# Performance work log

Hardware: AMD Instinct MI355X
Metric: run time of the kernel (lower is better)

The kernel has to match this reference:

```python
import jax, jax.numpy as jnp
import numpy as np

D_IN = 1024
D_OUT = 1024
NUM_HEADS = 16
HEAD_DIM = D_OUT // NUM_HEADS


def setup_inputs() -> dict:
    key = jax.random.key(0)
    ks = jax.random.split(key, 6)
    scale = 0.02
    x = jax.random.normal(ks[0], (4, 2048, D_IN), dtype=jnp.float32)
    Wq = jax.random.normal(ks[1], (D_IN, D_OUT), dtype=jnp.float32) * scale
    Wk = jax.random.normal(ks[2], (D_IN, D_OUT), dtype=jnp.float32) * scale
    Wv = jax.random.normal(ks[3], (D_IN, D_OUT), dtype=jnp.float32) * scale
    Wo = jax.random.normal(ks[4], (D_OUT, D_OUT), dtype=jnp.float32) * scale
    bo = jax.random.normal(ks[5], (D_OUT,), dtype=jnp.float32) * scale
    return {"x": x, "Wq": Wq, "Wk": Wk, "Wv": Wv, "Wo": Wo, "bo": bo}


def reference(x, Wq, Wk, Wv, Wo, bo):
    b, n, _ = x.shape
    # QKV projections -> [b, h, n, hd]
    def split_heads(t):
        return t.reshape(b, n, NUM_HEADS, HEAD_DIM).transpose(0, 2, 1, 3)
    q = split_heads(x @ Wq)
    k = split_heads(x @ Wk)
    v = split_heads(x @ Wv)
    # scaled causal attention scores [b, h, n, n]
    scores = jnp.einsum('bhqd,bhkd->bhqk', q, k) / jnp.sqrt(jnp.float32(HEAD_DIM))
    causal = jnp.tril(jnp.ones((n, n), dtype=bool))
    scores = jnp.where(causal, scores, -jnp.inf)
    attn = jax.nn.softmax(scores, axis=-1)
    # dropout p=0.0 -> identity
    ctx = jnp.einsum('bhqk,bhkd->bhqd', attn, v)  # [b, h, n, hd]
    ctx = ctx.transpose(0, 2, 1, 3).reshape(b, n, D_OUT)
    return ctx @ Wo + bo
```

## Files before the change

### kernel.cpp

```cpp
#include <hip/hip_runtime.h>
#include <hip/hip_bf16.h>

typedef __bf16 bf16;
typedef __attribute__((ext_vector_type(8))) __bf16 bf16x8;
typedef __attribute__((ext_vector_type(4))) __bf16 bf16x4;
typedef __attribute__((ext_vector_type(4))) float floatx4;

#define DM 1024
#define NH 16
#define HD 64
#define SEQ 2048
#define BATCH 4
#define MTOT (BATCH * SEQ)

#define GLDS(g, l) \
  __builtin_amdgcn_global_load_lds((const __attribute__((address_space(1))) void*)(g), \
                                   (__attribute__((address_space(3))) void*)(l), 16, 0, 0)

__global__ void cvt_f32_bf16(const float* __restrict__ in, bf16* __restrict__ out, int n4) {
  int i = blockIdx.x * 256 + threadIdx.x;
  if (i < n4) {
    float4 v = ((const float4*)in)[i];
    bf16x4 o;
    o[0] = (bf16)v.x; o[1] = (bf16)v.y; o[2] = (bf16)v.z; o[3] = (bf16)v.w;
    ((bf16x4*)out)[i] = o;
  }
}

__global__ void transpose_cvt4(const float* __restrict__ Wq, const float* __restrict__ Wk,
                               const float* __restrict__ Wv, const float* __restrict__ Wo,
                               bf16* __restrict__ Wqkvt, bf16* __restrict__ Wot) {
  __shared__ float tile[32][33];
  const float* W;
  bf16* Wt;
  int z = blockIdx.z;
  if (z == 0) { W = Wq; Wt = Wqkvt; }
  else if (z == 1) { W = Wk; Wt = Wqkvt + (size_t)DM * DM; }
  else if (z == 2) { W = Wv; Wt = Wqkvt + (size_t)2 * DM * DM; }
  else { W = Wo; Wt = Wot; }
  int n0 = blockIdx.x * 32, k0 = blockIdx.y * 32;
  int tx = threadIdx.x, ty = threadIdx.y;
#pragma unroll
  for (int j = 0; j < 32; j += 8)
    tile[ty + j][tx] = W[(size_t)(k0 + ty + j) * DM + n0 + tx];
  __syncthreads();
#pragma unroll
  for (int j = 0; j < 32; j += 8)
    Wt[(size_t)(n0 + ty + j) * DM + k0 + tx] = (bf16)tile[tx][ty + j];
}

#define BK 64

__global__ __launch_bounds__(256, 3) void gemm_qkv(const bf16* __restrict__ A,
                                                   const bf16* __restrict__ Bt,
                                                   bf16* __restrict__ Qb,
                                                   bf16* __restrict__ Kb,
                                                   bf16* __restrict__ Vt) {
  __shared__ __align__(16) bf16 Alds[128 * BK];
  __shared__ __align__(16) bf16 Blds[128 * BK];
  const int K = 1024;
  int m0 = blockIdx.x * 128;
  int n0 = blockIdx.y * 128;
  int tid = threadIdx.x;
  int wave = tid >> 6, lane = tid & 63;
  int wm = (wave & 1) * 64, wn = (wave >> 1) * 64;
  int lm = lane & 15, quad = lane >> 4;
  int lm7 = lm & 7;

  int cbase = wave * 64 + lane;
  const bf16* gA[4];
  const bf16* gB[4];
  bf16 *lA[4], *lB[4];
#pragma unroll
  for (int seg = 0; seg < 4; ++seg) {
    int c = seg * 256 + cbase;
    int row = c >> 3;
    int col8 = (c & 7) ^ (row & 7);
    gA[seg] = A + (size_t)(m0 + row) * K + col8 * 8;
    gB[seg] = Bt + (size_t)(n0 + row) * K + col8 * 8;
    lA[seg] = Alds + c * 8;
    lB[seg] = Blds + c * 8;
  }

  floatx4 acc[4][4] = {};
  for (int kt = 0; kt < K; kt += BK) {
    __syncthreads();
#pragma unroll
    for (int seg = 0; seg < 4; ++seg) {
      GLDS(gA[seg] + kt, lA[seg]);
      GLDS(gB[seg] + kt, lB[seg]);
    }
    __syncthreads();
#pragma unroll
    for (int ks = 0; ks < 2; ++ks) {
      int xk = (ks * 4 + quad) ^ lm7;
      bf16x8 af[4], bfr[4];
#pragma unroll
      for (int t = 0; t < 4; ++t) {
        af[t] = *(const bf16x8*)(Alds + (wm + t * 16 + lm) * BK + xk * 8);
        bfr[t] = *(const bf16x8*)(Blds + (wn + t * 16 + lm) * BK + xk * 8);
      }
#pragma unroll
      for (int i = 0; i < 4; ++i)
#pragma unroll
        for (int j = 0; j < 4; ++j)
          acc[i][j] = __builtin_amdgcn_mfma_f32_16x16x32_bf16(af[i], bfr[j], acc[i][j], 0, 0, 0);
    }
  }
#pragma unroll
  for (int i = 0; i < 4; ++i) {
#pragma unroll
    for (int j = 0; j < 4; ++j) {
#pragma unroll
      for (int r = 0; r < 4; ++r) {
        int R = m0 + wm + i * 16 + quad * 4 + r;
        int C = n0 + wn + j * 16 + lm;
        int b = R >> 11, n = R & 2047;
        int proj = C >> 10, c = C & 1023;
        int h = c >> 6, d = c & 63;
        int bh = b * NH + h;
        bf16 bv = (bf16)acc[i][j][r];
        if (proj == 0)
          Qb[((size_t)bh * SEQ + n) * HD + d] = bv;
        else if (proj == 1)
          Kb[((size_t)bh * SEQ + n) * HD + d] = bv;
        else
          Vt[((size_t)bh * HD + d) * SEQ + n] = bv;
      }
    }
  }
}

__global__ __launch_bounds__(256, 3) void gemm_out(const bf16* __restrict__ A,
                                                   const bf16* __restrict__ Bt,
                                                   const float* __restrict__ bias,
                                                   float* __restrict__ out) {
  __shared__ __align__(16) bf16 Alds[128 * BK];
  __shared__ __align__(16) bf16 Blds[128 * BK];
  const int K = 1024;
  int m0 = blockIdx.x * 128;
  int n0 = blockIdx.y * 128;
  int tid = threadIdx.x;
  int wave = tid >> 6, lane = tid & 63;
  int wm = (wave & 1) * 64, wn = (wave >> 1) * 64;
  int lm = lane & 15, quad = lane >> 4;
  int lm7 = lm & 7;

  int cbase = wave * 64 + lane;
  const bf16* gA[4];
  const bf16* gB[4];
  bf16 *lA[4], *lB[4];
#pragma unroll
  for (int seg = 0; seg < 4; ++seg) {
    int c = seg * 256 + cbase;
    int row = c >> 3;
    int col8 = (c & 7) ^ (row & 7);
    gA[seg] = A + (size_t)(m0 + row) * K + col8 * 8;
    gB[seg] = Bt + (size_t)(n0 + row) * K + col8 * 8;
    lA[seg] = Alds + c * 8;
    lB[seg] = Blds + c * 8;
  }

  floatx4 acc[4][4] = {};
  for (int kt = 0; kt < K; kt += BK) {
    __syncthreads();
#pragma unroll
    for (int seg = 0; seg < 4; ++seg) {
      GLDS(gA[seg] + kt, lA[seg]);
      GLDS(gB[seg] + kt, lB[seg]);
    }
    __syncthreads();
#pragma unroll
    for (int ks = 0; ks < 2; ++ks) {
      int xk = (ks * 4 + quad) ^ lm7;
      bf16x8 af[4], bfr[4];
#pragma unroll
      for (int t = 0; t < 4; ++t) {
        af[t] = *(const bf16x8*)(Alds + (wm + t * 16 + lm) * BK + xk * 8);
        bfr[t] = *(const bf16x8*)(Blds + (wn + t * 16 + lm) * BK + xk * 8);
      }
#pragma unroll
      for (int i = 0; i < 4; ++i)
#pragma unroll
        for (int j = 0; j < 4; ++j)
          acc[i][j] = __builtin_amdgcn_mfma_f32_16x16x32_bf16(af[i], bfr[j], acc[i][j], 0, 0, 0);
    }
  }
#pragma unroll
  for (int i = 0; i < 4; ++i)
#pragma unroll
    for (int j = 0; j < 4; ++j)
#pragma unroll
      for (int r = 0; r < 4; ++r) {
        int R = m0 + wm + i * 16 + quad * 4 + r;
        int C = n0 + wn + j * 16 + lm;
        out[(size_t)R * DM + C] = acc[i][j][r] + bias[C];
      }
}

__global__ __launch_bounds__(256) void attn(const bf16* __restrict__ Qb,
                                            const bf16* __restrict__ Kb,
                                            const bf16* __restrict__ Vt,
                                            bf16* __restrict__ ctx) {
  __shared__ __align__(16) bf16 Klds[64 * 64];
  __shared__ __align__(16) bf16 Vlds[64 * 64];
  int blk = blockIdx.x;
  int xcd = blk & 7;
  int idx = blk >> 3;
  int bh = (idx & 7) * 8 + xcd;
  int pr = idx >> 3;
  int tid = threadIdx.x, wave = tid >> 6, lane = tid & 63;
  int lm = lane & 15, quad = lane >> 4;
  int lm7 = lm & 7;
  const bf16* Qp = Qb + (size_t)bh * SEQ * HD;
  const bf16* Kp = Kb + (size_t)bh * SEQ * HD;
  const bf16* Vp = Vt + (size_t)bh * HD * SEQ;
  int b = bh >> 4, h = bh & 15;
  const float QSCALE = 0.125f * 1.4426950408889634f;

  int c1 = tid, c2 = tid + 256;
  int r1 = c1 >> 3, l1 = (c1 & 7) ^ (r1 & 7);
  int r2 = c2 >> 3, l2 = (c2 & 7) ^ (r2 & 7);
  const bf16* Kg1 = Kp + (size_t)r1 * HD + l1 * 8;
  const bf16* Kg2 = Kp + (size_t)r2 * HD + l2 * 8;
  const bf16* Vg1 = Vp + (size_t)r1 * SEQ + (l1 >> 2) * 32 + (l1 & 3) * 4;
  const bf16* Vg2 = Vp + (size_t)r2 * SEQ + (l2 >> 2) * 32 + (l2 & 3) * 4;

  bf16x8 ones;
#pragma unroll
  for (int j = 0; j < 8; ++j) ones[j] = (lm == 0) ? (bf16)1.0f : (bf16)0.0f;

  int xk0 = (quad ^ lm7) * 8;
  int xk1 = ((4 + quad) ^ lm7) * 8;

#pragma unroll 1
  for (int half = 0; half < 2; ++half) {
    int qt = half ? pr : 15 - pr;
    int q0 = qt * 128;
    int rowbase = q0 + wave * 32;
    int nkv = 2 * qt + 2;

    bf16x8 qfA[2], qfB[2];
#pragma unroll
    for (int ks2 = 0; ks2 < 2; ++ks2) {
      bf16x8 qa = *(const bf16x8*)(Qp + (size_t)(rowbase + lm) * HD + ks2 * 32 + quad * 8);
      bf16x8 qb = *(const bf16x8*)(Qp + (size_t)(rowbase + 16 + lm) * HD + ks2 * 32 + quad * 8);
#pragma unroll
      for (int j = 0; j < 8; ++j) {
        qa[j] = (bf16)((float)qa[j] * QSCALE);
        qb[j] = (bf16)((float)qb[j] * QSCALE);
      }
      qfA[ks2] = qa;
      qfB[ks2] = qb;
    }

    floatx4 accA[4] = {}, accB[4] = {};
    floatx4 aclA = {}, aclB = {};

    if (half) __syncthreads();

    bf16x8 k1 = *(const bf16x8*)Kg1;
    bf16x8 k2 = *(const bf16x8*)Kg2;
    bf16x4 v1a = *(const bf16x4*)Vg1, v1b = *(const bf16x4*)(Vg1 + 16);
    bf16x4 v2a = *(const bf16x4*)Vg2, v2b = *(const bf16x4*)(Vg2 + 16);
    *(bf16x8*)(Klds + c1 * 8) = k1;
    *(bf16x8*)(Klds + c2 * 8) = k2;
    *(bf16x4*)(Vlds + c1 * 8) = v1a;
    *(bf16x4*)(Vlds + c1 * 8 + 4) = v1b;
    *(bf16x4*)(Vlds + c2 * 8) = v2a;
    *(bf16x4*)(Vlds + c2 * 8 + 4) = v2b;

#pragma unroll 1
    for (int t = 0; t < nkv; ++t) {
      __syncthreads();
      int kv0 = t * 64;
      if (t + 1 < nkv) {
        int kn = kv0 + 64;
        k1 = *(const bf16x8*)(Kg1 + (size_t)kn * HD);
        k2 = *(const bf16x8*)(Kg2 + (size_t)kn * HD);
        v1a = *(const bf16x4*)(Vg1 + kn);
        v1b = *(const bf16x4*)(Vg1 + kn + 16);
        v2a = *(const bf16x4*)(Vg2 + kn);
        v2b = *(const bf16x4*)(Vg2 + kn + 16);
      }

      if (kv0 <= rowbase + 31) {
        floatx4 stA[4] = {}, stB[4] = {};
#pragma unroll
        for (int mt = 0; mt < 4; ++mt) {
          const bf16* kr = Klds + (mt * 16 + lm) * 64;
          bf16x8 kf0 = *(const bf16x8*)(kr + xk0);
          bf16x8 kf1 = *(const bf16x8*)(kr + xk1);
          stA[mt] = __builtin_amdgcn_mfma_f32_16x16x32_bf16(kf0, qfA[0], stA[mt], 0, 0, 0);
          stA[mt] = __builtin_amdgcn_mfma_f32_16x16x32_bf16(kf1, qfA[1], stA[mt], 0, 0, 0);
          stB[mt] = __builtin_amdgcn_mfma_f32_16x16x32_bf16(kf0, qfB[0], stB[mt], 0, 0, 0);
          stB[mt] = __builtin_amdgcn_mfma_f32_16x16x32_bf16(kf1, qfB[1], stB[mt], 0, 0, 0);
        }

        bf16x8 pfA2[2], pfB2[2];
        if (kv0 + 63 <= rowbase) {
#pragma unroll
          for (int mt = 0; mt < 4; ++mt)
#pragma unroll
            for (int r = 0; r < 4; ++r) {
              pfA2[mt >> 1][(mt & 1) * 4 + r] = (bf16)exp2f(stA[mt][r]);
              pfB2[mt >> 1][(mt & 1) * 4 + r] = (bf16)exp2f(stB[mt][r]);
            }
        } else {
          int qrelA = rowbase - kv0 + lm;
          int qrelB = qrelA + 16;
#pragma unroll
          for (int mt = 0; mt < 4; ++mt)
#pragma unroll
            for (int r = 0; r < 4; ++r) {
              int kvrel = mt * 16 + quad * 4 + r;
              float pa = exp2f(stA[mt][r]);
              float pbv = exp2f(stB[mt][r]);
              if (kvrel > qrelA) pa = 0.f;
              if (kvrel > qrelB) pbv = 0.f;
              pfA2[mt >> 1][(mt & 1) * 4 + r] = (bf16)pa;
              pfB2[mt >> 1][(mt & 1) * 4 + r] = (bf16)pbv;
            }
        }

#pragma unroll
        for (int ks = 0; ks < 2; ++ks) {
          int xv = ks ? xk1 : xk0;
          aclA = __builtin_amdgcn_mfma_f32_16x16x32_bf16(ones, pfA2[ks], aclA, 0, 0, 0);
          aclB = __builtin_amdgcn_mfma_f32_16x16x32_bf16(ones, pfB2[ks], aclB, 0, 0, 0);
#pragma unroll
          for (int db = 0; db < 4; ++db) {
            bf16x8 vf = *(const bf16x8*)(Vlds + (db * 16 + lm) * 64 + xv);
            accA[db] = __builtin_amdgcn_mfma_f32_16x16x32_bf16(vf, pfA2[ks], accA[db], 0, 0, 0);
            accB[db] = __builtin_amdgcn_mfma_f32_16x16x32_bf16(vf, pfB2[ks], accB[db], 0, 0, 0);
          }
        }
      }

      if (t + 1 < nkv) {
        __syncthreads();
        *(bf16x8*)(Klds + c1 * 8) = k1;
        *(bf16x8*)(Klds + c2 * 8) = k2;
        *(bf16x4*)(Vlds + c1 * 8) = v1a;
        *(bf16x4*)(Vlds + c1 * 8 + 4) = v1b;
        *(bf16x4*)(Vlds + c2 * 8) = v2a;
        *(bf16x4*)(Vlds + c2 * 8 + 4) = v2b;
      }
    }

    float linvA = 1.0f / __shfl(aclA[0], lm, 64);
    float linvB = 1.0f / __shfl(aclB[0], lm, 64);

    bf16* crowA = ctx + ((size_t)b * SEQ + rowbase + lm) * DM + h * 64;
    bf16* crowB = crowA + (size_t)16 * DM;
#pragma unroll
    for (int db = 0; db < 4; ++db) {
      bf16x4 oa, ob;
#pragma unroll
      for (int r = 0; r < 4; ++r) {
        oa[r] = (bf16)(accA[db][r] * linvA);
        ob[r] = (bf16)(accB[db][r] * linvB);
      }
      *(bf16x4*)(crowA + db * 16 + quad * 4) = oa;
      *(bf16x4*)(crowB + db * 16 + quad * 4) = ob;
    }
  }
}

extern "C" void kernel_launch(void* const* d_in, const int* in_sizes, int n_in,
                              void* d_out, int out_size, void* d_ws, size_t ws_size,
                              hipStream_t stream) {
  const float* x = (const float*)d_in[0];
  const float* Wq = (const float*)d_in[1];
  const float* Wk = (const float*)d_in[2];
  const float* Wv = (const float*)d_in[3];
  const float* Wo = (const float*)d_in[4];
  const float* bo = (const float*)d_in[5];
  float* out = (float*)d_out;

  bf16* ws = (bf16*)d_ws;
  bf16* xb = ws;
  bf16* Wqkvt = xb + (size_t)MTOT * DM;
  bf16* Wot = Wqkvt + (size_t)3 * DM * DM;
  bf16* Qb = Wot + (size_t)DM * DM;
  bf16* Kb = Qb + (size_t)BATCH * NH * SEQ * HD;
  bf16* Vtb = Kb + (size_t)BATCH * NH * SEQ * HD;
  bf16* ctx = xb;

  cvt_f32_bf16<<<(MTOT * DM / 4 + 255) / 256, 256, 0, stream>>>(x, xb, MTOT * DM / 4);
  transpose_cvt4<<<dim3(32, 32, 4), dim3(32, 8), 0, stream>>>(Wq, Wk, Wv, Wo, Wqkvt, Wot);
  gemm_qkv<<<dim3(MTOT / 128, 3 * DM / 128), 256, 0, stream>>>(xb, Wqkvt, Qb, Kb, Vtb);
  attn<<<512, 256, 0, stream>>>(Qb, Kb, Vtb, ctx);
  gemm_out<<<dim3(MTOT / 128, DM / 128), 256, 0, stream>>>(ctx, Wot, bo, out);
}
```

Before: 257.6 us.

## Split attention KV loop across two wave groups with LDS reduction

```diff
diff --git a/kernel.cpp b/kernel.cpp
--- a/kernel.cpp
+++ b/kernel.cpp
@@ -12,6 +12,12 @@
 #define SEQ 2048
 #define BATCH 4
 #define MTOT (BATCH * SEQ)
+
+#if __has_builtin(__builtin_amdgcn_exp2f)
+#define EXP2(x) __builtin_amdgcn_exp2f(x)
+#else
+#define EXP2(x) exp2f(x)
+#endif
 
 #define GLDS(g, l) \
   __builtin_amdgcn_global_load_lds((const __attribute__((address_space(1))) void*)(g), \
@@ -198,18 +204,18 @@
       }
 }
 
-__global__ __launch_bounds__(256) void attn(const bf16* __restrict__ Qb,
-                                            const bf16* __restrict__ Kb,
-                                            const bf16* __restrict__ Vt,
-                                            bf16* __restrict__ ctx) {
-  __shared__ __align__(16) bf16 Klds[64 * 64];
-  __shared__ __align__(16) bf16 Vlds[64 * 64];
+__global__ __launch_bounds__(512, 4) void attn(const bf16* __restrict__ Qb,
+                                               const bf16* __restrict__ Kb,
+                                               const bf16* __restrict__ Vt,
+                                               bf16* __restrict__ ctx) {
+  __shared__ __align__(16) bf16 KV[4][4096];
   int blk = blockIdx.x;
   int xcd = blk & 7;
   int idx = blk >> 3;
   int bh = (idx & 7) * 8 + xcd;
   int pr = idx >> 3;
   int tid = threadIdx.x, wave = tid >> 6, lane = tid & 63;
+  int qg = wave & 3, par = wave >> 2;
   int lm = lane & 15, quad = lane >> 4;
   int lm7 = lm & 7;
   const bf16* Qp = Qb + (size_t)bh * SEQ * HD;
@@ -218,13 +224,13 @@
   int b = bh >> 4, h = bh & 15;
   const float QSCALE = 0.125f * 1.4426950408889634f;
 
-  int c1 = tid, c2 = tid + 256;
-  int r1 = c1 >> 3, l1 = (c1 & 7) ^ (r1 & 7);
-  int r2 = c2 >> 3, l2 = (c2 & 7) ^ (r2 & 7);
-  const bf16* Kg1 = Kp + (size_t)r1 * HD + l1 * 8;
-  const bf16* Kg2 = Kp + (size_t)r2 * HD + l2 * 8;
-  const bf16* Vg1 = Vp + (size_t)r1 * SEQ + (l1 >> 2) * 32 + (l1 & 3) * 4;
-  const bf16* Vg2 = Vp + (size_t)r2 * SEQ + (l2 >> 2) * 32 + (l2 & 3) * 4;
+  int c = tid;
+  int r = c >> 3, l = (c & 7) ^ (r & 7);
+  const bf16* Kg = Kp + (size_t)r * HD + l * 8;
+  const bf16* Vg = Vp + (size_t)r * SEQ + (l >> 2) * 32 + (l & 3) * 4;
+
+  const bf16* Kl = KV[par];
+  const bf16* Vl = KV[2 + par];
 
   bf16x8 ones;
 #pragma unroll
@@ -232,13 +238,16 @@
 
   int xk0 = (quad ^ lm7) * 8;
   int xk1 = ((4 + quad) ^ lm7) * 8;
+
+  float* cbuf = (float*)&KV[0][0];
+  int cb = qg * 1088 + lane;
 
 #pragma unroll 1
   for (int half = 0; half < 2; ++half) {
     int qt = half ? pr : 15 - pr;
     int q0 = qt * 128;
-    int rowbase = q0 + wave * 32;
-    int nkv = 2 * qt + 2;
+    int rowbase = q0 + qg * 32;
+    int ns = qt + 1;
 
     bf16x8 qfA[2], qfB[2];
 #pragma unroll
@@ -259,36 +268,32 @@
 
     if (half) __syncthreads();
 
-    bf16x8 k1 = *(const bf16x8*)Kg1;
-    bf16x8 k2 = *(const bf16x8*)Kg2;
-    bf16x4 v1a = *(const bf16x4*)Vg1, v1b = *(const bf16x4*)(Vg1 + 16);
-    bf16x4 v2a = *(const bf16x4*)Vg2, v2b = *(const bf16x4*)(Vg2 + 16);
-    *(bf16x8*)(Klds + c1 * 8) = k1;
-    *(bf16x8*)(Klds + c2 * 8) = k2;
-    *(bf16x4*)(Vlds + c1 * 8) = v1a;
-    *(bf16x4*)(Vlds + c1 * 8 + 4) = v1b;
-    *(bf16x4*)(Vlds + c2 * 8) = v2a;
-    *(bf16x4*)(Vlds + c2 * 8 + 4) = v2b;
+    bf16x8 kr0 = *(const bf16x8*)(Kg);
+    bf16x8 kr1 = *(const bf16x8*)(Kg + (size_t)64 * HD);
+    bf16x4 v0a = *(const bf16x4*)(Vg),      v0b = *(const bf16x4*)(Vg + 16);
+    bf16x4 v1a = *(const bf16x4*)(Vg + 64), v1b = *(const bf16x4*)(Vg + 80);
+    *(bf16x8*)(KV[0] + c * 8) = kr0;
+    *(bf16x8*)(KV[1] + c * 8) = kr1;
+    *(bf16x4*)(KV[2] + c * 8) = v0a; *(bf16x4*)(KV[2] + c * 8 + 4) = v0b;
+    *(bf16x4*)(KV[3] + c * 8) = v1a; *(bf16x4*)(KV[3] + c * 8 + 4) = v1b;
 
 #pragma unroll 1
-    for (int t = 0; t < nkv; ++t) {
+    for (int s = 0; s < ns; ++s) {
       __syncthreads();
-      int kv0 = t * 64;
-      if (t + 1 < nkv) {
-        int kn = kv0 + 64;
-        k1 = *(const bf16x8*)(Kg1 + (size_t)kn * HD);
-        k2 = *(const bf16x8*)(Kg2 + (size_t)kn * HD);
-        v1a = *(const bf16x4*)(Vg1 + kn);
-        v1b = *(const bf16x4*)(Vg1 + kn + 16);
-        v2a = *(const bf16x4*)(Vg2 + kn);
-        v2b = *(const bf16x4*)(Vg2 + kn + 16);
-      }
+      if (s + 1 < ns) {
+        int kt = (2 * s + 2) * 64;
+        kr0 = *(const bf16x8*)(Kg + (size_t)kt * HD);
+        kr1 = *(const bf16x8*)(Kg + (size_t)(kt + 64) * HD);
+        v0a = *(const bf16x4*)(Vg + kt);      v0b = *(const bf16x4*)(Vg + kt + 16);
+        v1a = *(const bf16x4*)(Vg + kt + 64); v1b = *(const bf16x4*)(Vg + kt + 80);
+      }
+      int kv0 = (2 * s + par) * 64;
 
       if (kv0 <= rowbase + 31) {
         floatx4 stA[4] = {}, stB[4] = {};
 #pragma unroll
         for (int mt = 0; mt < 4; ++mt) {
-          const bf16* kr = Klds + (mt * 16 + lm) * 64;
+          const bf16* kr = Kl + (mt * 16 + lm) * 64;
           bf16x8 kf0 = *(const bf16x8*)(kr + xk0);
           bf16x8 kf1 = *(const bf16x8*)(kr + xk1);
           stA[mt] = __builtin_amdgcn_mfma_f32_16x16x32_bf16(kf0, qfA[0], stA[mt], 0, 0, 0);
@@ -302,9 +307,9 @@
 #pragma unroll
           for (int mt = 0; mt < 4; ++mt)
 #pragma unroll
-            for (int r = 0; r < 4; ++r) {
-              pfA2[mt >> 1][(mt & 1) * 4 + r] = (bf16)exp2f(stA[mt][r]);
-              pfB2[mt >> 1][(mt & 1) * 4 + r] = (bf16)exp2f(stB[mt][r]);
+            for (int rr = 0; rr < 4; ++rr) {
+              pfA2[mt >> 1][(mt & 1) * 4 + rr] = (bf16)EXP2(stA[mt][rr]);
+              pfB2[mt >> 1][(mt & 1) * 4 + rr] = (bf16)EXP2(stB[mt][rr]);
             }
         } else {
           int qrelA = rowbase - kv0 + lm;
@@ -312,14 +317,14 @@
 #pragma unroll
           for (int mt = 0; mt < 4; ++mt)
 #pragma unroll
-            for (int r = 0; r < 4; ++r) {
-              int kvrel = mt * 16 + quad * 4 + r;
-              float pa = exp2f(stA[mt][r]);
-              float pbv = exp2f(stB[mt][r]);
+            for (int rr = 0; rr < 4; ++rr) {
+              int kvrel = mt * 16 + quad * 4 + rr;
+              float pa = EXP2(stA[mt][rr]);
+              float pbv = EXP2(stB[mt][rr]);
               if (kvrel > qrelA) pa = 0.f;
               if (kvrel > qrelB) pbv = 0.f;
-              pfA2[mt >> 1][(mt & 1) * 4 + r] = (bf16)pa;
-              pfB2[mt >> 1][(mt & 1) * 4 + r] = (bf16)pbv;
+              pfA2[mt >> 1][(mt & 1) * 4 + rr] = (bf16)pa;
+              pfB2[mt >> 1][(mt & 1) * 4 + rr] = (bf16)pbv;
             }
         }
 
@@ -330,39 +335,75 @@
           aclB = __builtin_amdgcn_mfma_f32_16x16x32_bf16(ones, pfB2[ks], aclB, 0, 0, 0);
 #pragma unroll
           for (int db = 0; db < 4; ++db) {
-            bf16x8 vf = *(const bf16x8*)(Vlds + (db * 16 + lm) * 64 + xv);
+            bf16x8 vf = *(const bf16x8*)(Vl + (db * 16 + lm) * 64 + xv);
             accA[db] = __builtin_amdgcn_mfma_f32_16x16x32_bf16(vf, pfA2[ks], accA[db], 0, 0, 0);
             accB[db] = __builtin_amdgcn_mfma_f32_16x16x32_bf16(vf, pfB2[ks], accB[db], 0, 0, 0);
           }
         }
       }
 
-      if (t + 1 < nkv) {
+      if (s + 1 < ns) {
         __syncthreads();
-        *(bf16x8*)(Klds + c1 * 8) = k1;
-        *(bf16x8*)(Klds + c2 * 8) = k2;
-        *(bf16x4*)(Vlds + c1 * 8) = v1a;
-        *(bf16x4*)(Vlds + c1 * 8 + 4) = v1b;
-        *(bf16x4*)(Vlds + c2 * 8) = v2a;
-        *(bf16x4*)(Vlds + c2 * 8 + 4) = v2b;
-      }
-    }
-
-    float linvA = 1.0f / __shfl(aclA[0], lm, 64);
-    float linvB = 1.0f / __shfl(aclB[0], lm, 64);
-
-    bf16* crowA = ctx + ((size_t)b * SEQ + rowbase + lm) * DM + h * 64;
-    bf16* crowB = crowA + (size_t)16 * DM;
-#pragma unroll
-    for (int db = 0; db < 4; ++db) {
-      bf16x4 oa, ob;
-#pragma unroll
-      for (int r = 0; r < 4; ++r) {
-        oa[r] = (bf16)(accA[db][r] * linvA);
-        ob[r] = (bf16)(accB[db][r] * linvB);
-      }
-      *(bf16x4*)(crowA + db * 16 + quad * 4) = oa;
-      *(bf16x4*)(crowB + db * 16 + quad * 4) = ob;
+        *(bf16x8*)(KV[0] + c * 8) = kr0;
+        *(bf16x8*)(KV[1] + c * 8) = kr1;
+        *(bf16x4*)(KV[2] + c * 8) = v0a; *(bf16x4*)(KV[2] + c * 8 + 4) = v0b;
+        *(bf16x4*)(KV[3] + c * 8) = v1a; *(bf16x4*)(KV[3] + c * 8 + 4) = v1b;
+      }
+    }
+
+    __syncthreads();
+    if (par) {
+#pragma unroll
+      for (int db = 0; db < 4; ++db)
+#pragma unroll
+        for (int rr = 0; rr < 4; ++rr)
+          cbuf[cb + (db * 4 + rr) * 64] = accA[db][rr];
+      cbuf[cb + 1024] = aclA[0];
+    }
+    __syncthreads();
+    float aA = aclA[0], aB = aclB[0];
+    if (!par) {
+#pragma unroll
+      for (int db = 0; db < 4; ++db)
+#pragma unroll
+        for (int rr = 0; rr < 4; ++rr)
+          accA[db][rr] += cbuf[cb + (db * 4 + rr) * 64];
+      aA += cbuf[cb + 1024];
+    }
+    __syncthreads();
+    if (par) {
+#pragma unroll
+      for (int db = 0; db < 4; ++db)
+#pragma unroll
+        for (int rr = 0; rr < 4; ++rr)
+          cbuf[cb + (db * 4 + rr) * 64] = accB[db][rr];
+      cbuf[cb + 1024] = aclB[0];
+    }
+    __syncthreads();
+    if (!par) {
+#pragma unroll
+      for (int db = 0; db < 4; ++db)
+#pragma unroll
+        for (int rr = 0; rr < 4; ++rr)
+          accB[db][rr] += cbuf[cb + (db * 4 + rr) * 64];
+      aB += cbuf[cb + 1024];
+
+      float linvA = 1.0f / __shfl(aA, lm, 64);
+      float linvB = 1.0f / __shfl(aB, lm, 64);
+
+      bf16* crowA = ctx + ((size_t)b * SEQ + rowbase + lm) * DM + h * 64;
+      bf16* crowB = crowA + (size_t)16 * DM;
+#pragma unroll
+      for (int db = 0; db < 4; ++db) {
+        bf16x4 oa, ob;
+#pragma unroll
+        for (int rr = 0; rr < 4; ++rr) {
+          oa[rr] = (bf16)(accA[db][rr] * linvA);
+          ob[rr] = (bf16)(accB[db][rr] * linvB);
+        }
+        *(bf16x4*)(crowA + db * 16 + quad * 4) = oa;
+        *(bf16x4*)(crowB + db * 16 + quad * 4) = ob;
+      }
     }
   }
 }
@@ -390,6 +431,6 @@
   cvt_f32_bf16<<<(MTOT * DM / 4 + 255) / 256, 256, 0, stream>>>(x, xb, MTOT * DM / 4);
   transpose_cvt4<<<dim3(32, 32, 4), dim3(32, 8), 0, stream>>>(Wq, Wk, Wv, Wo, Wqkvt, Wot);
   gemm_qkv<<<dim3(MTOT / 128, 3 * DM / 128), 256, 0, stream>>>(xb, Wqkvt, Qb, Kb, Vtb);
-  attn<<<512, 256, 0, stream>>>(Qb, Kb, Vtb, ctx);
+  attn<<<512, 512, 0, stream>>>(Qb, Kb, Vtb, ctx);
   gemm_out<<<dim3(MTOT / 128, DM / 128), 256, 0, stream>>>(ctx, Wot, bo, out);
 }
```

New measurement: 322.6 us. +25.3%, slower.
